# Optimization experiments

Hardware: AMD Instinct MI355X
Metric: run time of the kernel (lower is better)

Reference implementation:

```python
import jax, jax.numpy as jnp
import numpy as np

D_MODEL = 1024
D_STATE = 128
D_CONV = 4
EXPAND = 2
HEADDIM = 64
NGROUPS = 1
CHUNK = 256
D_INNER = EXPAND * D_MODEL          # 2048
NHEADS = D_INNER // HEADDIM         # 32
D_IN_PROJ = 2 * D_INNER + 2 * NGROUPS * D_STATE + NHEADS  # 4384
CONV_DIM = D_INNER + 2 * NGROUPS * D_STATE                # 2304
BATCH, SEQLEN = 2, 2048


def rmsnorm(x, w, eps=1e-6):
    ms = jnp.mean(x * x, axis=-1, keepdims=True)
    return w * (x * jax.lax.rsqrt(ms + eps))


def layernorm(x, eps=1e-5):
    mu = jnp.mean(x, axis=-1, keepdims=True)
    var = jnp.mean((x - mu) ** 2, axis=-1, keepdims=True)
    return (x - mu) * jax.lax.rsqrt(var + eps)


def activation_quant(x):
    # int8-style fake quant with STE, scale differentiable (matches torch)
    amax = jnp.clip(jnp.max(jnp.abs(x), axis=-1, keepdims=True), 1e-5, None)
    scale = 127.0 / amax
    q = jnp.clip(jnp.round(x * scale), -128, 127)
    return (jax.lax.stop_gradient(q - x * scale) + x * scale) / scale


def weight_quant(w):
    # ternary {-1,0,1}; note: NOT rescaled by scale (matches the triton kernel)
    scale = jnp.clip(jnp.mean(jnp.abs(w)), 1e-5, None)
    wq = jnp.clip(jnp.round(w / scale), -1.0, 1.0)
    return w + jax.lax.stop_gradient(wq - w)  # STE: identity grad


def bitlinear(x, w):
    return activation_quant(layernorm(x)) @ weight_quant(w).T


def segsum(x):
    # x: [..., T] -> [..., T, T] lower-triangular cumulative segment sums
    T = x.shape[-1]
    cs = jnp.cumsum(x, axis=-1)
    ss = cs[..., :, None] - cs[..., None, :]
    mask = jnp.tril(jnp.ones((T, T), dtype=bool))
    return jnp.where(mask, ss, -jnp.inf)


def ssd(u, a, B, C, chunk):
    # u: b l h p (= x*dt); a: b l h (= A*dt); B, C: b l h n (per-head)
    b, l, h, p = u.shape
    n = B.shape[-1]
    c = l // chunk
    u = u.reshape(b, c, chunk, h, p)
    a = a.reshape(b, c, chunk, h).transpose(0, 3, 1, 2)   # b h c s
    B = B.reshape(b, c, chunk, h, n)
    C = C.reshape(b, c, chunk, h, n)
    a_cs = jnp.cumsum(a, axis=-1)                          # b h c s
    L = jnp.exp(segsum(a))                                 # b h c s s
    Y_diag = jnp.einsum('bclhn,bcshn,bhcls,bcshp->bclhp', C, B, L, u)
    decay_states = jnp.exp(a_cs[..., -1:] - a_cs)          # b h c s
    states = jnp.einsum('bclhn,bhcl,bclhp->bchpn', B, decay_states, u)
    a_chunk = jnp.pad(a_cs[..., -1], ((0, 0), (0, 0), (1, 0)))  # b h (c+1)
    decay_chunk = jnp.exp(segsum(a_chunk))                 # b h (c+1) (c+1)
    states = jnp.concatenate([jnp.zeros_like(states[:, :1]), states], axis=1)
    new_states = jnp.einsum('bhzc,bchpn->bzhpn', decay_chunk, states)
    prev_states = new_states[:, :-1]                       # state entering each chunk
    Y_off = jnp.einsum('bclhn,bchpn,bhcl->bclhp', C, prev_states, jnp.exp(a_cs))
    return (Y_diag + Y_off).reshape(b, l, h, p)


def setup_inputs() -> dict:
    key = jax.random.key(0)
    ks = jax.random.split(key, 6)
    hidden_states = jax.random.normal(ks[0], (BATCH, SEQLEN, D_MODEL), jnp.float32)
    in_proj_w = jax.random.normal(ks[1], (D_IN_PROJ, D_MODEL), jnp.float32) / np.sqrt(D_MODEL).astype(np.float32)
    out_proj_w = jax.random.normal(ks[2], (D_MODEL, D_INNER), jnp.float32) / np.sqrt(D_INNER).astype(np.float32)
    conv_w = jax.random.normal(ks[3], (CONV_DIM, D_CONV), jnp.float32) * 0.1
    conv_b = jnp.zeros((CONV_DIM,), jnp.float32)
    A_log = jnp.log(jnp.arange(1, NHEADS + 1, dtype=jnp.float32))
    Dp = jnp.ones((NHEADS,), jnp.float32)
    dt_min, dt_max, dt_floor = 1e-3, 1e-1, 1e-4
    inv_dt = jnp.exp(jax.random.uniform(ks[4], (NHEADS,)) * (np.log(dt_max) - np.log(dt_min)) + np.log(dt_min))
    inv_dt = jnp.clip(inv_dt, dt_floor, None)
    dt_bias = inv_dt + jnp.log(-jnp.expm1(-inv_dt))
    norm_w = jnp.ones((D_MODEL,), jnp.float32)
    out_norm_w = jnp.ones((D_INNER,), jnp.float32)
    return dict(hidden_states=hidden_states, norm_w=norm_w, in_proj_w=in_proj_w,
                conv_w=conv_w, conv_b=conv_b, A_log=A_log, Dp=Dp, dt_bias=dt_bias,
                out_norm_w=out_norm_w, out_proj_w=out_proj_w)


def reference(hidden_states, norm_w, in_proj_w, conv_w, conv_b, A_log, Dp, dt_bias, out_norm_w, out_proj_w):
    b, l, _ = hidden_states.shape
    h = rmsnorm(hidden_states, norm_w)
    zxbcdt = bitlinear(h, in_proj_w)                       # b l (2*d_inner + 2*g*n + h)
    z = zxbcdt[..., :D_INNER]
    xBC = zxbcdt[..., D_INNER:D_INNER + CONV_DIM]
    dt = zxbcdt[..., D_INNER + CONV_DIM:]                  # b l h
    # causal depthwise conv1d (kernel D_CONV) + silu
    xp = jnp.pad(xBC, ((0, 0), (D_CONV - 1, 0), (0, 0)))
    conv = sum(xp[:, k:k + l, :] * conv_w[:, k] for k in range(D_CONV)) + conv_b
    xBC = jax.nn.silu(conv)
    x = xBC[..., :D_INNER].reshape(b, l, NHEADS, HEADDIM)
    Bm = xBC[..., D_INNER:D_INNER + NGROUPS * D_STATE].reshape(b, l, NGROUPS, D_STATE)
    Cm = xBC[..., D_INNER + NGROUPS * D_STATE:].reshape(b, l, NGROUPS, D_STATE)
    hpg = NHEADS // NGROUPS
    Bh = jnp.repeat(Bm, hpg, axis=2)                       # b l h n
    Ch = jnp.repeat(Cm, hpg, axis=2)
    dt = jax.nn.softplus(dt + dt_bias)                     # dt_softplus=True
    A = -jnp.exp(A_log)
    y = ssd(x * dt[..., None], dt * A, Bh, Ch, CHUNK)      # b l h p
    y = y + x * Dp[None, None, :, None]                    # D skip
    y = y * jax.nn.silu(z).reshape(b, l, NHEADS, HEADDIM)  # z gate
    y = rmsnorm(y.reshape(b, l, D_INNER), out_norm_w)
    out = bitlinear(y, out_proj_w)
    return hidden_states + out
```

## Files before the change

### kernel.cpp

```cpp
#include <hip/hip_runtime.h>
#include <stdint.h>
#include <stddef.h>
#include <math.h>

#define TOKS 4096
#define DM   1024
#define DIP  4384
#define DI   2048
#define CVD  2304
#define NH   32
#define HD   64
#define DST  128
#define NCH  8
#define CHK  256

typedef int v4i  __attribute__((ext_vector_type(4)));
typedef int v16i __attribute__((ext_vector_type(16)));
typedef short s8v __attribute__((ext_vector_type(8)));
typedef float f16v __attribute__((ext_vector_type(16)));
typedef unsigned short ushort_t;

static const size_t OFF_ZX    = 0;
static const size_t OFF_SX    = OFF_ZX + (size_t)TOKS*DIP*4;
static const size_t OFF_ST    = OFF_SX + (size_t)TOKS*CVD*4;
static const size_t OFF_YG    = OFF_ST + (size_t)512*HD*DST*4;
static const size_t OFF_Q1    = OFF_YG + (size_t)TOKS*DI*4;
static const size_t OFF_Q2    = OFF_Q1 + (size_t)TOKS*DM;
static const size_t OFF_WQ1   = OFF_Q2 + (size_t)TOKS*DI;
static const size_t OFF_WQ2   = OFF_WQ1 + (size_t)DIP*DM;
static const size_t OFF_RS1   = OFF_WQ2 + (size_t)DM*DI;
static const size_t OFF_RS2   = OFF_RS1 + (size_t)TOKS*4;
static const size_t OFF_DT    = OFF_RS2 + (size_t)TOKS*4;
static const size_t OFF_ACS   = OFF_DT + (size_t)TOKS*NH*4;
static const size_t OFF_CSUM  = OFF_ACS + (size_t)512*CHK*8;
static const size_t OFF_PART  = OFF_CSUM + 512*8;
static const size_t OFF_WSC   = OFF_PART + 1024*8;
static const size_t OFF_BH    = OFF_WSC + 64;
static const size_t OFF_BL    = OFF_BH  + (size_t)TOKS*128*2;
static const size_t OFF_CHG   = OFF_BL  + (size_t)TOKS*128*2;
static const size_t OFF_CLG   = OFF_CHG + (size_t)TOKS*128*2;
static const size_t OFF_GRAM  = OFF_CLG + (size_t)TOKS*128*2;
static const size_t OFF_UTH   = OFF_GRAM + (size_t)16*256*256*4;
static const size_t OFF_UTL   = OFF_UTH + (size_t)512*64*256*2;
static const size_t OFF_PH    = OFF_UTL + (size_t)512*64*256*2;
static const size_t OFF_PL    = OFF_PH  + (size_t)512*64*128*2;

__device__ __forceinline__ ushort_t f2bf(float x) {
  union { float f; unsigned int u; } v; v.f = x;
  unsigned int r = v.u + 0x7FFFu + ((v.u >> 16) & 1u);
  return (ushort_t)(r >> 16);
}
__device__ __forceinline__ float bf2f(ushort_t h) {
  union { unsigned int u; float f; } v; v.u = ((unsigned int)h) << 16;
  return v.f;
}

__device__ __forceinline__ double bsumd(double v, double* sb) {
#pragma unroll
  for (int o = 32; o; o >>= 1) v += __shfl_down(v, o);
  int lane = threadIdx.x & 63, w = threadIdx.x >> 6;
  __syncthreads();
  if (lane == 0) sb[w] = v;
  __syncthreads();
  return sb[0] + sb[1] + sb[2] + sb[3];
}
__device__ __forceinline__ double bmaxd(double v, double* sb) {
#pragma unroll
  for (int o = 32; o; o >>= 1) v = fmax(v, __shfl_down(v, o));
  int lane = threadIdx.x & 63, w = threadIdx.x >> 6;
  __syncthreads();
  if (lane == 0) sb[w] = v;
  __syncthreads();
  return fmax(fmax(sb[0], sb[1]), fmax(sb[2], sb[3]));
}
__device__ __forceinline__ void bsum3d(double& a, double& b, double& c, double* sb) {
#pragma unroll
  for (int o = 32; o; o >>= 1) {
    a += __shfl_down(a, o);
    b += __shfl_down(b, o);
    c += __shfl_down(c, o);
  }
  int lane = threadIdx.x & 63, w = threadIdx.x >> 6;
  __syncthreads();
  if (lane == 0) { sb[w * 3 + 0] = a; sb[w * 3 + 1] = b; sb[w * 3 + 2] = c; }
  __syncthreads();
  a = sb[0] + sb[3] + sb[6] + sb[9];
  b = sb[1] + sb[4] + sb[7] + sb[10];
  c = sb[2] + sb[5] + sb[8] + sb[11];
}

__global__ void __launch_bounds__(256) k_absmean(const float* __restrict__ w, int n, double* __restrict__ part) {
  double s = 0.0;
  for (int i = blockIdx.x * 256 + threadIdx.x; i < n; i += 512 * 256) s += (double)fabsf(w[i]);
  __shared__ double sb[4];
  s = bsumd(s, sb);
  if (threadIdx.x == 0) part[blockIdx.x] = s;
}

__global__ void __launch_bounds__(256) k_wscale(const double* __restrict__ part, double* __restrict__ wsc, int n1, int n2) {
  __shared__ double sb[4];
  double s = part[threadIdx.x] + part[threadIdx.x + 256];
  double t1 = bsumd(s, sb);
  __syncthreads();
  s = part[512 + threadIdx.x] + part[512 + threadIdx.x + 256];
  double t2 = bsumd(s, sb);
  if (threadIdx.x == 0) {
    wsc[0] = fmax(t1 / (double)n1, 1e-5);
    wsc[1] = fmax(t2 / (double)n2, 1e-5);
  }
}

__global__ void __launch_bounds__(256) k_tern(const float* __restrict__ w, int n, const double* __restrict__ wsc, int which, int8_t* __restrict__ out) {
  int i = blockIdx.x * 256 + threadIdx.x;
  if (i < n) {
    double sc = wsc[which];
    double q = fmin(fmax(rint((double)w[i] / sc), -1.0), 1.0);
    out[i] = (int8_t)q;
  }
}

template <int D>
__global__ void __launch_bounds__(256) k_normquant(const float* __restrict__ in, const float* __restrict__ w,
                                                   int8_t* __restrict__ q, float* __restrict__ rs) {
  constexpr int E = D / 256;
  int t = blockIdx.x, tid = threadIdx.x;
  const float* row = in + (size_t)t * D;
  __shared__ double sb[12];
  double y[E];
  double s0 = 0.0, s1 = 0.0, s2 = 0.0;
#pragma unroll
  for (int i = 0; i < E; i++) {
    double xv = (double)row[tid + 256 * i];
    double wv = (double)w[tid + 256 * i];
    s0 += xv * xv;
    double yy = wv * xv;
    y[i] = yy;
    s1 += yy;
    s2 += yy * yy;
  }
  bsum3d(s0, s1, s2, sb);
  double rr = 1.0 / sqrt(s0 / (double)D + 1e-6);
  double mu = rr * (s1 / (double)D);
  double var = rr * rr * (s2 / (double)D) - mu * mu;
  double rv = 1.0 / sqrt(var + 1e-5);
  double M = 0.0;
#pragma unroll
  for (int i = 0; i < E; i++) { y[i] = y[i] * rr - mu; M = fmax(M, fabs(y[i])); }
  M = bmaxd(M, sb);
  double am = fmax(M * rv, 1e-5);
  double sc = 127.0 / am;
#pragma unroll
  for (int i = 0; i < E; i++) {
    double qq = fmin(fmax(rint(y[i] * rv * sc), -128.0), 127.0);
    q[(size_t)t * D + tid + 256 * i] = (int8_t)qq;
  }
  if (tid == 0) rs[t] = (float)(am / 127.0);
}

__global__ void __launch_bounds__(256, 3) k_gemm_mfma(const int8_t* __restrict__ A, const int8_t* __restrict__ W,
                                                      const float* __restrict__ rs, const float* __restrict__ addend,
                                                      float* __restrict__ out, int M, int N, int K) {
  __shared__ int8_t Al[128 * 80];
  __shared__ int8_t Bl[128 * 80];
  int m0 = blockIdx.x * 128, n0 = blockIdx.y * 128;
  int t = threadIdx.x;
  int w = t >> 6, lane = t & 63;
  int wm = w >> 1, wn = w & 1;
  int l31 = lane & 31, lh = lane >> 5;

  v16i acc[2][2] = {};

  for (int k0 = 0; k0 < K; k0 += 64) {
    __syncthreads();
#pragma unroll
    for (int it = 0; it < 2; ++it) {
      int c = t + 256 * it;
      int row = c >> 2, kc = (c & 3) * 16;
      int4 av = *(const int4*)(A + (size_t)(m0 + row) * K + k0 + kc);
      *(int4*)(Al + row * 80 + kc) = av;
      int4 bv;
      if (n0 + row < N) bv = *(const int4*)(W + (size_t)(n0 + row) * K + k0 + kc);
      else { bv.x = bv.y = bv.z = bv.w = 0; }
      *(int4*)(Bl + row * 80 + kc) = bv;
    }
    __syncthreads();
#pragma unroll
    for (int ks = 0; ks < 2; ++ks) {
      v4i af[2], bf[2];
#pragma unroll
      for (int tm = 0; tm < 2; ++tm)
        af[tm] = *(const v4i*)(Al + (wm * 64 + tm * 32 + l31) * 80 + ks * 32 + lh * 16);
#pragma unroll
      for (int tn = 0; tn < 2; ++tn)
        bf[tn] = *(const v4i*)(Bl + (wn * 64 + tn * 32 + l31) * 80 + ks * 32 + lh * 16);
#pragma unroll
      for (int tm = 0; tm < 2; ++tm)
#pragma unroll
        for (int tn = 0; tn < 2; ++tn)
          acc[tm][tn] = __builtin_amdgcn_mfma_i32_32x32x32_i8(af[tm], bf[tn], acc[tm][tn], 0, 0, 0);
    }
  }

#pragma unroll
  for (int tm = 0; tm < 2; ++tm)
#pragma unroll
    for (int tn = 0; tn < 2; ++tn) {
      int n = n0 + wn * 64 + tn * 32 + l31;
      if (n < N) {
#pragma unroll
        for (int r = 0; r < 16; ++r) {
          int mrel = (r & 3) + 8 * (r >> 2) + 4 * lh;
          int m = m0 + wm * 64 + tm * 32 + mrel;
          float v = rs[m] * (float)acc[tm][tn][r];
          if (addend) v += addend[(size_t)m * N + n];
          out[(size_t)m * N + n] = v;
        }
      }
    }
}

__global__ void __launch_bounds__(256) k_conv(const float* __restrict__ zx, const float* __restrict__ cw,
                                              const float* __restrict__ cb, float* __restrict__ sx,
                                              ushort_t* __restrict__ bh, ushort_t* __restrict__ bl,
                                              ushort_t* __restrict__ ch, ushort_t* __restrict__ cl) {
  int c = blockIdx.x * 256 + threadIdx.x;
  int t = blockIdx.y;
  int b = t >> 11, l = t & 2047;
  float acc = cb[c];
#pragma unroll
  for (int k = 0; k < 4; k++) {
    int li = l - 3 + k;
    if (li >= 0) acc = fmaf(zx[(size_t)(b * 2048 + li) * DIP + DI + c], cw[c * 4 + k], acc);
  }
  float val = acc / (1.f + expf(-acc));
  sx[(size_t)t * CVD + c] = val;
  if (c >= DI) {
    int idx = c - DI;
    ushort_t hh = f2bf(val);
    ushort_t ll = f2bf(val - bf2f(hh));
    if (idx < 128) {
      bh[(size_t)t * 128 + idx] = hh;
      bl[(size_t)t * 128 + idx] = ll;
    } else {
      ch[(size_t)t * 128 + idx - 128] = hh;
      cl[(size_t)t * 128 + idx - 128] = ll;
    }
  }
}

__global__ void __launch_bounds__(256) k_dt(const float* __restrict__ zx, const float* __restrict__ dt_bias,
                                            float* __restrict__ dtv) {
  int idx = blockIdx.x * 256 + threadIdx.x;
  int t = idx >> 5, h = idx & 31;
  float x = zx[(size_t)t * DIP + (DI + CVD) + h] + dt_bias[h];
  dtv[idx] = fmaxf(x, 0.f) + log1pf(expf(-fabsf(x)));
}

__global__ void __launch_bounds__(256) k_cumsum(const float* __restrict__ dtv, const float* __restrict__ A_log,
                                                double* __restrict__ acs, double* __restrict__ csum) {
  int bid = blockIdx.x;
  int h = bid & 31, bc = bid >> 5;
  int s = threadIdx.x;
  int tok = bc * 256 + s;
  double negA = -exp((double)A_log[h]);
  double a = (double)dtv[tok * 32 + h] * negA;
  __shared__ double buf[256];
  buf[s] = a;
  __syncthreads();
  for (int o = 1; o < 256; o <<= 1) {
    double add = (s >= o) ? buf[s - o] : 0.0;
    __syncthreads();
    buf[s] += add;
    __syncthreads();
  }
  acs[(size_t)bid * 256 + s] = buf[s];
  if (s == 255) csum[bid] = buf[s];
}

__global__ void __launch_bounds__(256) k_gram(const ushort_t* __restrict__ bhg, const ushort_t* __restrict__ blg,
                                              const ushort_t* __restrict__ chg, const ushort_t* __restrict__ clg,
                                              float* __restrict__ gram) {
  int blk = blockIdx.x;
  int bc = blk >> 3, lt = blk & 7;
  int t = threadIdx.x;
  int w = t >> 6, lane = t & 63;
  int l31 = lane & 31, lhf = lane >> 5;
  __shared__ float Gl[4][32 * 36];

  s8v ch[8], cl[8];
  size_t tokA = (size_t)(bc * 256 + lt * 32 + l31) * 128;
#pragma unroll
  for (int ks = 0; ks < 8; ++ks) {
    ch[ks] = *(const s8v*)(chg + tokA + ks * 16 + lhf * 8);
    cl[ks] = *(const s8v*)(clg + tokA + ks * 16 + lhf * 8);
  }
  for (int st = w; st <= lt; st += 4) {
    size_t tokB = (size_t)(bc * 256 + st * 32 + l31) * 128;
    f16v acc = {};
#pragma unroll
    for (int ks = 0; ks < 8; ++ks) {
      s8v bh = *(const s8v*)(bhg + tokB + ks * 16 + lhf * 8);
      s8v bl = *(const s8v*)(blg + tokB + ks * 16 + lhf * 8);
      acc = __builtin_amdgcn_mfma_f32_32x32x16_bf16(ch[ks], bh, acc, 0, 0, 0);
      acc = __builtin_amdgcn_mfma_f32_32x32x16_bf16(ch[ks], bl, acc, 0, 0, 0);
      acc = __builtin_amdgcn_mfma_f32_32x32x16_bf16(cl[ks], bh, acc, 0, 0, 0);
    }
#pragma unroll
    for (int rr = 0; rr < 16; ++rr) {
      int lrow = (rr & 3) + 8 * (rr >> 2) + 4 * lhf;
      Gl[w][lrow * 36 + l31] = acc[rr];
    }
    int lr = lane >> 1, c0 = (lane & 1) * 16;
    float* gdst = gram + ((size_t)bc * 256 + lt * 32 + lr) * 256 + st * 32 + c0;
#pragma unroll
    for (int i = 0; i < 4; ++i)
      *(float4*)(gdst + i * 4) = *(const float4*)(&Gl[w][lr * 36 + c0 + i * 4]);
  }
}

__global__ void __launch_bounds__(256) k_prepuT(const float* __restrict__ sx, const float* __restrict__ dtv,
                                                ushort_t* __restrict__ uth, ushort_t* __restrict__ utl) {
  int r = blockIdx.x;
  int h = r & 31, bc = r >> 5;
  int t = threadIdx.x;
  __shared__ float Xs[64 * 68];
  __shared__ float dts[64];
  for (int slab = 0; slab < 4; ++slab) {
    int s0 = slab * 64;
    if (slab) __syncthreads();
    if (t < 64) dts[t] = dtv[(size_t)(bc * 256 + s0 + t) * 32 + h];
    {
      int s = t >> 2, pg = (t & 3) * 16;
      const float* xr = sx + (size_t)(bc * 256 + s0 + s) * CVD + h * 64 + pg;
      float* dst = &Xs[s * 68 + pg];
#pragma unroll
      for (int i = 0; i < 4; ++i)
        *(float4*)(dst + i * 4) = *(const float4*)(xr + i * 4);
    }
    __syncthreads();
    {
      int p = t >> 2, sg = (t & 3) * 16;
      union { int4 q[2]; ushort_t e[16]; } H, L;
#pragma unroll
      for (int j = 0; j < 16; ++j) {
        float f = Xs[(sg + j) * 68 + p] * dts[sg + j];
        ushort_t hh = f2bf(f);
        H.e[j] = hh;
        L.e[j] = f2bf(f - bf2f(hh));
      }
      size_t base = ((size_t)r * 64 + p) * 256 + s0 + sg;
      *(int4*)(uth + base) = H.q[0];
      *(int4*)(uth + base + 8) = H.q[1];
      *(int4*)(utl + base) = L.q[0];
      *(int4*)(utl + base + 8) = L.q[1];
    }
  }
}

__global__ void __launch_bounds__(256, 4) k_states2(const float* __restrict__ sx, const float* __restrict__ dtv,
                                                    const double* __restrict__ acs, const double* __restrict__ csum,
                                                    float* __restrict__ states) {
  int r = blockIdx.x;
  int h = r & 31, bc = r >> 5;
  int t = threadIdx.x, tx = t & 15, ty = t >> 4;
  __shared__ float du[64 * 68];
  double last = csum[r];
  float acc[4][8] = {};
  for (int s0 = 0; s0 < 256; s0 += 64) {
    __syncthreads();
    {
      int s = t >> 2, pg = (t & 3) * 16;
      int tok = bc * 256 + s0 + s;
      float w = expf((float)(last - acs[(size_t)r * 256 + s0 + s])) * dtv[(size_t)tok * 32 + h];
      const float* xr = sx + (size_t)tok * CVD + h * 64 + pg;
      float* dst = &du[s * 68 + pg];
#pragma unroll
      for (int i = 0; i < 4; i++) {
        float4 v = *(const float4*)(xr + i * 4);
        v.x *= w; v.y *= w; v.z *= w; v.w *= w;
        *(float4*)(dst + i * 4) = v;
      }
    }
    __syncthreads();
#pragma unroll 4
    for (int s = 0; s < 64; s++) {
      int tok = bc * 256 + s0 + s;
      const float* br = sx + (size_t)tok * CVD + DI + ty * 8;
      float4 b0 = *(const float4*)(br);
      float4 b1 = *(const float4*)(br + 4);
      float4 d4 = *(const float4*)(&du[s * 68 + tx * 4]);
      float dd[4] = {d4.x, d4.y, d4.z, d4.w};
      float bv[8] = {b0.x, b0.y, b0.z, b0.w, b1.x, b1.y, b1.z, b1.w};
#pragma unroll
      for (int i = 0; i < 4; i++)
#pragma unroll
        for (int j = 0; j < 8; j++) acc[i][j] = fmaf(dd[i], bv[j], acc[i][j]);
    }
  }
  size_t base = (size_t)r * (HD * DST);
#pragma unroll
  for (int i = 0; i < 4; i++) {
    float4 v0, v1;
    v0.x = acc[i][0]; v0.y = acc[i][1]; v0.z = acc[i][2]; v0.w = acc[i][3];
    v1.x = acc[i][4]; v1.y = acc[i][5]; v1.z = acc[i][6]; v1.w = acc[i][7];
    *(float4*)(states + base + (size_t)(tx * 4 + i) * DST + ty * 8) = v0;
    *(float4*)(states + base + (size_t)(tx * 4 + i) * DST + ty * 8 + 4) = v1;
  }
}

__global__ void __launch_bounds__(256) k_chunkscan(float* __restrict__ states, const double* __restrict__ csum,
                                                   ushort_t* __restrict__ ph, ushort_t* __restrict__ pl) {
  int idx = blockIdx.x * 256 + threadIdx.x;
  int n = idx & 127, p = (idx >> 7) & 63, h = (idx >> 13) & 31, b = idx >> 18;
  float Nv = 0.f;
  for (int c = 0; c < 8; c++) {
    int bid = (b * 8 + c) * 32 + h;
    size_t addr = (size_t)bid * (HD * DST) + p * DST + n;
    float s = states[addr];
    states[addr] = Nv;
    ushort_t hh = f2bf(Nv);
    ph[addr] = hh;
    pl[addr] = f2bf(Nv - bf2f(hh));
    Nv = Nv * expf((float)csum[bid]) + s;
  }
}

__global__ void __launch_bounds__(64) k_y8(const float* __restrict__ sx, const double* __restrict__ acs,
                                           const ushort_t* __restrict__ chg, const ushort_t* __restrict__ clg,
                                           const ushort_t* __restrict__ prevh, const ushort_t* __restrict__ prevl,
                                           const float* __restrict__ gram,
                                           const ushort_t* __restrict__ uth, const ushort_t* __restrict__ utl,
                                           const float* __restrict__ zx, const float* __restrict__ Dp,
                                           float* __restrict__ yg) {
  int myid = (blockIdx.x & 7) * 512 + (blockIdx.x >> 3);
  int r = myid >> 3, lt = myid & 7;
  int h = r & 31, bc = r >> 5;
  int lane = threadIdx.x;
  int l31 = lane & 31, lhf = lane >> 5;
  int lw = lt * 32;
  int lg = lw + l31;
  const double* acsr = acs + (size_t)r * 256;
  double a_l = acsr[lg];

  f16v Yacc[2] = {};
  {
    size_t ca = (size_t)(bc * 256 + lg) * 128;
#pragma unroll
    for (int ks = 0; ks < 8; ++ks) {
      s8v ch = *(const s8v*)(chg + ca + ks * 16 + lhf * 8);
      s8v cl = *(const s8v*)(clg + ca + ks * 16 + lhf * 8);
#pragma unroll
      for (int pt = 0; pt < 2; ++pt) {
        size_t pa = ((size_t)r * 64 + pt * 32 + l31) * 128 + ks * 16 + lhf * 8;
        s8v ph = *(const s8v*)(prevh + pa);
        s8v pl = *(const s8v*)(prevl + pa);
        Yacc[pt] = __builtin_amdgcn_mfma_f32_32x32x16_bf16(ch, ph, Yacc[pt], 0, 0, 0);
        Yacc[pt] = __builtin_amdgcn_mfma_f32_32x32x16_bf16(ch, pl, Yacc[pt], 0, 0, 0);
        Yacc[pt] = __builtin_amdgcn_mfma_f32_32x32x16_bf16(cl, ph, Yacc[pt], 0, 0, 0);
      }
    }
  }
#pragma unroll
  for (int rr = 0; rr < 16; ++rr) {
    int lrow = (rr & 3) + 8 * (rr >> 2) + 4 * lhf;
    float el = expf((float)acsr[lw + lrow]);
    Yacc[0][rr] *= el;
    Yacc[1][rr] *= el;
  }

  const float* gbase = gram + (size_t)(bc * 256 + lg) * 256;
  size_t ub0 = ((size_t)r * 64 + l31) * 256;
  size_t ub1 = ((size_t)r * 64 + 32 + l31) * 256;

  s8v AH[2], AL[2], UH[4], UL[4];
  {
#pragma unroll
    for (int k2 = 0; k2 < 2; ++k2) {
      int sb = k2 * 16 + lhf * 8;
      float4 g0 = *(const float4*)(gbase + sb);
      float4 g1 = *(const float4*)(gbase + sb + 4);
      float gv[8] = {g0.x, g0.y, g0.z, g0.w, g1.x, g1.y, g1.z, g1.w};
      union { s8v v; ushort_t e[8]; } H, L;
#pragma unroll
      for (int j = 0; j < 8; ++j) {
        float v = 0.f;
        if (sb + j <= lg) v = expf((float)(a_l - acsr[sb + j])) * gv[j];
        ushort_t hh = f2bf(v);
        H.e[j] = hh;
        L.e[j] = f2bf(v - bf2f(hh));
      }
      AH[k2] = H.v; AL[k2] = L.v;
      UH[k2 * 2 + 0] = *(const s8v*)(uth + ub0 + sb);
      UH[k2 * 2 + 1] = *(const s8v*)(uth + ub1 + sb);
      UL[k2 * 2 + 0] = *(const s8v*)(utl + ub0 + sb);
      UL[k2 * 2 + 1] = *(const s8v*)(utl + ub1 + sb);
    }
  }

  for (int st = 0; st <= lt; ++st) {
    float4 ng0[2], ng1[2];
    s8v nUH[4], nUL[4];
    bool more = (st < lt);
    int s1 = (st + 1) * 32;
    if (more) {
#pragma unroll
      for (int k2 = 0; k2 < 2; ++k2) {
        int sb = s1 + k2 * 16 + lhf * 8;
        ng0[k2] = *(const float4*)(gbase + sb);
        ng1[k2] = *(const float4*)(gbase + sb + 4);
        nUH[k2 * 2 + 0] = *(const s8v*)(uth + ub0 + sb);
        nUH[k2 * 2 + 1] = *(const s8v*)(uth + ub1 + sb);
        nUL[k2 * 2 + 0] = *(const s8v*)(utl + ub0 + sb);
        nUL[k2 * 2 + 1] = *(const s8v*)(utl + ub1 + sb);
      }
    }
    __builtin_amdgcn_s_setprio(1);
#pragma unroll
    for (int k2 = 0; k2 < 2; ++k2) {
#pragma unroll
      for (int pt = 0; pt < 2; ++pt) {
        Yacc[pt] = __builtin_amdgcn_mfma_f32_32x32x16_bf16(AH[k2], UH[k2 * 2 + pt], Yacc[pt], 0, 0, 0);
        Yacc[pt] = __builtin_amdgcn_mfma_f32_32x32x16_bf16(AH[k2], UL[k2 * 2 + pt], Yacc[pt], 0, 0, 0);
        Yacc[pt] = __builtin_amdgcn_mfma_f32_32x32x16_bf16(AL[k2], UH[k2 * 2 + pt], Yacc[pt], 0, 0, 0);
      }
    }
    __builtin_amdgcn_s_setprio(0);
    if (more) {
#pragma unroll
      for (int k2 = 0; k2 < 2; ++k2) {
        int sb = s1 + k2 * 16 + lhf * 8;
        float gv[8] = {ng0[k2].x, ng0[k2].y, ng0[k2].z, ng0[k2].w,
                       ng1[k2].x, ng1[k2].y, ng1[k2].z, ng1[k2].w};
        union { s8v v; ushort_t e[8]; } H, L;
#pragma unroll
        for (int j = 0; j < 8; ++j) {
          float v = 0.f;
          if (sb + j <= lg) v = expf((float)(a_l - acsr[sb + j])) * gv[j];
          ushort_t hh = f2bf(v);
          H.e[j] = hh;
          L.e[j] = f2bf(v - bf2f(hh));
        }
        AH[k2] = H.v; AL[k2] = L.v;
        UH[k2 * 2 + 0] = nUH[k2 * 2 + 0];
        UH[k2 * 2 + 1] = nUH[k2 * 2 + 1];
        UL[k2 * 2 + 0] = nUL[k2 * 2 + 0];
        UL[k2 * 2 + 1] = nUL[k2 * 2 + 1];
      }
    }
  }

  float dph = Dp[h];
#pragma unroll
  for (int pt = 0; pt < 2; ++pt) {
    int p = pt * 32 + l31;
#pragma unroll
    for (int rr = 0; rr < 16; ++rr) {
      int lrow = (rr & 3) + 8 * (rr >> 2) + 4 * lhf;
      size_t tok = (size_t)(bc * 256 + lw + lrow);
      float xv = sx[tok * CVD + h * 64 + p];
      float zv = zx[tok * DIP + h * 64 + p];
      float y = (Yacc[pt][rr] + xv * dph) * (zv / (1.f + expf(-zv)));
      yg[tok * DI + h * 64 + p] = y;
    }
  }
}

extern "C" void kernel_launch(void* const* d_in, const int* in_sizes, int n_in,
                              void* d_out, int out_size, void* d_ws, size_t ws_size,
                              hipStream_t stream) {
  const float* hidden   = (const float*)d_in[0];
  const float* norm_w   = (const float*)d_in[1];
  const float* in_proj  = (const float*)d_in[2];
  const float* conv_w   = (const float*)d_in[3];
  const float* conv_b   = (const float*)d_in[4];
  const float* A_log    = (const float*)d_in[5];
  const float* Dp       = (const float*)d_in[6];
  const float* dt_bias  = (const float*)d_in[7];
  const float* out_norm = (const float*)d_in[8];
  const float* out_proj = (const float*)d_in[9];
  float* out = (float*)d_out;

  char* ws = (char*)d_ws;
  float*  zx    = (float*)(ws + OFF_ZX);
  float*  sx    = (float*)(ws + OFF_SX);
  float*  st    = (float*)(ws + OFF_ST);
  float*  yg    = (float*)(ws + OFF_YG);
  int8_t* q1    = (int8_t*)(ws + OFF_Q1);
  int8_t* q2    = (int8_t*)(ws + OFF_Q2);
  int8_t* wq1   = (int8_t*)(ws + OFF_WQ1);
  int8_t* wq2   = (int8_t*)(ws + OFF_WQ2);
  float*  rs1   = (float*)(ws + OFF_RS1);
  float*  rs2   = (float*)(ws + OFF_RS2);
  float*  dtv   = (float*)(ws + OFF_DT);
  double* acs   = (double*)(ws + OFF_ACS);
  double* csum  = (double*)(ws + OFF_CSUM);
  double* part  = (double*)(ws + OFF_PART);
  double* wsc   = (double*)(ws + OFF_WSC);
  ushort_t* bhg = (ushort_t*)(ws + OFF_BH);
  ushort_t* blg = (ushort_t*)(ws + OFF_BL);
  ushort_t* chg = (ushort_t*)(ws + OFF_CHG);
  ushort_t* clg = (ushort_t*)(ws + OFF_CLG);
  float*  gram  = (float*)(ws + OFF_GRAM);
  ushort_t* uth = (ushort_t*)(ws + OFF_UTH);
  ushort_t* utl = (ushort_t*)(ws + OFF_UTL);
  ushort_t* pvh = (ushort_t*)(ws + OFF_PH);
  ushort_t* pvl = (ushort_t*)(ws + OFF_PL);

  const int n1 = DIP * DM, n2 = DM * DI;

  hipLaunchKernelGGL(k_absmean, dim3(512), dim3(256), 0, stream, in_proj, n1, part);
  hipLaunchKernelGGL(k_absmean, dim3(512), dim3(256), 0, stream, out_proj, n2, part + 512);
  hipLaunchKernelGGL(k_wscale, dim3(1), dim3(256), 0, stream, part, wsc, n1, n2);
  hipLaunchKernelGGL(k_tern, dim3((n1 + 255) / 256), dim3(256), 0, stream, in_proj, n1, wsc, 0, wq1);
  hipLaunchKernelGGL(k_tern, dim3((n2 + 255) / 256), dim3(256), 0, stream, out_proj, n2, wsc, 1, wq2);
  hipLaunchKernelGGL(k_normquant<DM>, dim3(TOKS), dim3(256), 0, stream, hidden, norm_w, q1, rs1);
  hipLaunchKernelGGL(k_gemm_mfma, dim3(TOKS / 128, (DIP + 127) / 128), dim3(256), 0, stream,
                     q1, wq1, rs1, (const float*)nullptr, zx, TOKS, DIP, DM);
  hipLaunchKernelGGL(k_conv, dim3(CVD / 256, TOKS), dim3(256), 0, stream, zx, conv_w, conv_b, sx,
                     bhg, blg, chg, clg);
  hipLaunchKernelGGL(k_dt, dim3(TOKS * NH / 256), dim3(256), 0, stream, zx, dt_bias, dtv);
  hipLaunchKernelGGL(k_cumsum, dim3(512), dim3(256), 0, stream, dtv, A_log, acs, csum);
  hipLaunchKernelGGL(k_gram, dim3(128), dim3(256), 0, stream, bhg, blg, chg, clg, gram);
  hipLaunchKernelGGL(k_prepuT, dim3(512), dim3(256), 0, stream, sx, dtv, uth, utl);
  hipLaunchKernelGGL(k_states2, dim3(512), dim3(256), 0, stream, sx, dtv, acs, csum, st);
  hipLaunchKernelGGL(k_chunkscan, dim3(2 * NH * HD * DST / 256), dim3(256), 0, stream, st, csum, pvh, pvl);
  hipLaunchKernelGGL(k_y8, dim3(4096), dim3(64), 0, stream, sx, acs, chg, clg, pvh, pvl, gram, uth, utl, zx, Dp, yg);
  hipLaunchKernelGGL(k_normquant<DI>, dim3(TOKS), dim3(256), 0, stream, yg, out_norm, q2, rs2);
  hipLaunchKernelGGL(k_gemm_mfma, dim3(TOKS / 128, DM / 128), dim3(256), 0, stream,
                     q2, wq2, rs2, hidden, out, TOKS, DM, DI);
  (void)in_sizes; (void)n_in; (void)out_size; (void)ws_size;
}
```

Measured before the change: 422.0 us.

## Store SSD operands in MFMA-fragment order and fold dt softplus into cumsum

The producers (conv, gram, prepuT, chunkscan) now write B/C, the Gram matrix, the transposed u and the previous-state operands in a layout that matches the per-lane MFMA fragment order. Each lane's loads in the gram and y kernels then fall in one contiguous 16-byte chunk and neighbouring lanes read neighbouring chunks, replacing strided row accesses. The dt softplus is fused into the cumsum kernel, which removes one launch and one pass over dt. The y kernel also drops its manual software prefetch and setprio scheduling in favour of a plain loop, which may expose more load latency.

```diff
diff --git a/kernel.cpp b/kernel.cpp
--- a/kernel.cpp
+++ b/kernel.cpp
@@ -221,8 +221,8 @@
 
 __global__ void __launch_bounds__(256) k_conv(const float* __restrict__ zx, const float* __restrict__ cw,
                                               const float* __restrict__ cb, float* __restrict__ sx,
-                                              ushort_t* __restrict__ bh, ushort_t* __restrict__ bl,
-                                              ushort_t* __restrict__ ch, ushort_t* __restrict__ cl) {
+                                              ushort_t* __restrict__ bh2, ushort_t* __restrict__ bl2,
+                                              ushort_t* __restrict__ ch2, ushort_t* __restrict__ cl2) {
   int c = blockIdx.x * 256 + threadIdx.x;
   int t = blockIdx.y;
   int b = t >> 11, l = t & 2047;
@@ -238,32 +238,27 @@
     int idx = c - DI;
     ushort_t hh = f2bf(val);
     ushort_t ll = f2bf(val - bf2f(hh));
-    if (idx < 128) {
-      bh[(size_t)t * 128 + idx] = hh;
-      bl[(size_t)t * 128 + idx] = ll;
-    } else {
-      ch[(size_t)t * 128 + idx - 128] = hh;
-      cl[(size_t)t * 128 + idx - 128] = ll;
-    }
-  }
-}
-
-__global__ void __launch_bounds__(256) k_dt(const float* __restrict__ zx, const float* __restrict__ dt_bias,
-                                            float* __restrict__ dtv) {
-  int idx = blockIdx.x * 256 + threadIdx.x;
-  int t = idx >> 5, h = idx & 31;
-  float x = zx[(size_t)t * DIP + (DI + CVD) + h] + dt_bias[h];
-  dtv[idx] = fmaxf(x, 0.f) + log1pf(expf(-fabsf(x)));
-}
-
-__global__ void __launch_bounds__(256) k_cumsum(const float* __restrict__ dtv, const float* __restrict__ A_log,
+    int bc = t >> 8, lt = (t >> 5) & 7, l31 = t & 31;
+    int n = idx & 127;
+    int ks = n >> 4, lhf = (n >> 3) & 1, j = n & 7;
+    size_t o = ((((size_t)(bc * 8 + lt) * 8 + ks) * 2 + lhf) * 32 + l31) * 8 + j;
+    if (idx < 128) { bh2[o] = hh; bl2[o] = ll; }
+    else           { ch2[o] = hh; cl2[o] = ll; }
+  }
+}
+
+__global__ void __launch_bounds__(256) k_cumsum(const float* __restrict__ zx, const float* __restrict__ dt_bias,
+                                                const float* __restrict__ A_log, float* __restrict__ dtv,
                                                 double* __restrict__ acs, double* __restrict__ csum) {
   int bid = blockIdx.x;
   int h = bid & 31, bc = bid >> 5;
   int s = threadIdx.x;
   int tok = bc * 256 + s;
+  float x = zx[(size_t)tok * DIP + (DI + CVD) + h] + dt_bias[h];
+  float dt = fmaxf(x, 0.f) + log1pf(expf(-fabsf(x)));
+  dtv[(size_t)tok * 32 + h] = dt;
   double negA = -exp((double)A_log[h]);
-  double a = (double)dtv[tok * 32 + h] * negA;
+  double a = (double)dt * negA;
   __shared__ double buf[256];
   buf[s] = a;
   __syncthreads();
@@ -277,9 +272,9 @@
   if (s == 255) csum[bid] = buf[s];
 }
 
-__global__ void __launch_bounds__(256) k_gram(const ushort_t* __restrict__ bhg, const ushort_t* __restrict__ blg,
-                                              const ushort_t* __restrict__ chg, const ushort_t* __restrict__ clg,
-                                              float* __restrict__ gram) {
+__global__ void __launch_bounds__(256) k_gram(const ushort_t* __restrict__ bh2, const ushort_t* __restrict__ bl2,
+                                              const ushort_t* __restrict__ ch2, const ushort_t* __restrict__ cl2,
+                                              float* __restrict__ gr2) {
   int blk = blockIdx.x;
   int bc = blk >> 3, lt = blk & 7;
   int t = threadIdx.x;
@@ -288,19 +283,19 @@
   __shared__ float Gl[4][32 * 36];
 
   s8v ch[8], cl[8];
-  size_t tokA = (size_t)(bc * 256 + lt * 32 + l31) * 128;
 #pragma unroll
   for (int ks = 0; ks < 8; ++ks) {
-    ch[ks] = *(const s8v*)(chg + tokA + ks * 16 + lhf * 8);
-    cl[ks] = *(const s8v*)(clg + tokA + ks * 16 + lhf * 8);
+    size_t ca = ((((size_t)(bc * 8 + lt) * 8 + ks) * 2 + lhf) * 32 + l31) * 8;
+    ch[ks] = *(const s8v*)(ch2 + ca);
+    cl[ks] = *(const s8v*)(cl2 + ca);
   }
   for (int st = w; st <= lt; st += 4) {
-    size_t tokB = (size_t)(bc * 256 + st * 32 + l31) * 128;
     f16v acc = {};
 #pragma unroll
     for (int ks = 0; ks < 8; ++ks) {
-      s8v bh = *(const s8v*)(bhg + tokB + ks * 16 + lhf * 8);
-      s8v bl = *(const s8v*)(blg + tokB + ks * 16 + lhf * 8);
+      size_t ba = ((((size_t)(bc * 8 + st) * 8 + ks) * 2 + lhf) * 32 + l31) * 8;
+      s8v bh = *(const s8v*)(bh2 + ba);
+      s8v bl = *(const s8v*)(bl2 + ba);
       acc = __builtin_amdgcn_mfma_f32_32x32x16_bf16(ch[ks], bh, acc, 0, 0, 0);
       acc = __builtin_amdgcn_mfma_f32_32x32x16_bf16(ch[ks], bl, acc, 0, 0, 0);
       acc = __builtin_amdgcn_mfma_f32_32x32x16_bf16(cl[ks], bh, acc, 0, 0, 0);
@@ -310,16 +305,21 @@
       int lrow = (rr & 3) + 8 * (rr >> 2) + 4 * lhf;
       Gl[w][lrow * 36 + l31] = acc[rr];
     }
-    int lr = lane >> 1, c0 = (lane & 1) * 16;
-    float* gdst = gram + ((size_t)bc * 256 + lt * 32 + lr) * 256 + st * 32 + c0;
-#pragma unroll
-    for (int i = 0; i < 4; ++i)
-      *(float4*)(gdst + i * 4) = *(const float4*)(&Gl[w][lr * 36 + c0 + i * 4]);
+#pragma unroll
+    for (int i2 = 0; i2 < 2; ++i2) {
+      int idx = i2 * 2 + lhf;
+      int k2g = idx >> 1, lhf2 = idx & 1;
+      size_t gb = ((((size_t)(bc * 8 + lt) * 8 + st) * 2 + k2g) * 2 + lhf2) * 256 + l31 * 8;
+      float4 a = *(const float4*)(&Gl[w][l31 * 36 + k2g * 16 + lhf2 * 8]);
+      float4 b = *(const float4*)(&Gl[w][l31 * 36 + k2g * 16 + lhf2 * 8 + 4]);
+      *(float4*)(gr2 + gb) = a;
+      *(float4*)(gr2 + gb + 4) = b;
+    }
   }
 }
 
 __global__ void __launch_bounds__(256) k_prepuT(const float* __restrict__ sx, const float* __restrict__ dtv,
-                                                ushort_t* __restrict__ uth, ushort_t* __restrict__ utl) {
+                                                ushort_t* __restrict__ uth2, ushort_t* __restrict__ utl2) {
   int r = blockIdx.x;
   int h = r & 31, bc = r >> 5;
   int t = threadIdx.x;
@@ -338,21 +338,25 @@
         *(float4*)(dst + i * 4) = *(const float4*)(xr + i * 4);
     }
     __syncthreads();
-    {
-      int p = t >> 2, sg = (t & 3) * 16;
-      union { int4 q[2]; ushort_t e[16]; } H, L;
-#pragma unroll
-      for (int j = 0; j < 16; ++j) {
-        float f = Xs[(sg + j) * 68 + p] * dts[sg + j];
+#pragma unroll
+    for (int half = 0; half < 2; ++half) {
+      int it = t + half * 256;
+      int l31 = it & 31, g = it >> 5;
+      int stl = g >> 3, k2 = (g >> 2) & 1, pt = (g >> 1) & 1, lhf = g & 1;
+      int p = pt * 32 + l31;
+      int sb = stl * 32 + k2 * 16 + lhf * 8;
+      union { int4 q; ushort_t e[8]; } H, L;
+#pragma unroll
+      for (int j = 0; j < 8; ++j) {
+        float f = Xs[(sb + j) * 68 + p] * dts[sb + j];
         ushort_t hh = f2bf(f);
         H.e[j] = hh;
         L.e[j] = f2bf(f - bf2f(hh));
       }
-      size_t base = ((size_t)r * 64 + p) * 256 + s0 + sg;
-      *(int4*)(uth + base) = H.q[0];
-      *(int4*)(uth + base + 8) = H.q[1];
-      *(int4*)(utl + base) = L.q[0];
-      *(int4*)(utl + base + 8) = L.q[1];
+      int st = slab * 2 + stl;
+      size_t base = (((((size_t)r * 8 + st) * 2 + k2) * 2 + pt) * 2 + lhf) * 256 + l31 * 8;
+      *(int4*)(uth2 + base) = H.q;
+      *(int4*)(utl2 + base) = L.q;
     }
   }
 }
@@ -409,9 +413,10 @@
 }
 
 __global__ void __launch_bounds__(256) k_chunkscan(float* __restrict__ states, const double* __restrict__ csum,
-                                                   ushort_t* __restrict__ ph, ushort_t* __restrict__ pl) {
+                                                   ushort_t* __restrict__ ph2, ushort_t* __restrict__ pl2) {
   int idx = blockIdx.x * 256 + threadIdx.x;
   int n = idx & 127, p = (idx >> 7) & 63, h = (idx >> 13) & 31, b = idx >> 18;
+  int ks = n >> 4, lhf = (n >> 3) & 1, j = n & 7, pt = p >> 5, l31 = p & 31;
   float Nv = 0.f;
   for (int c = 0; c < 8; c++) {
     int bid = (b * 8 + c) * 32 + h;
@@ -419,17 +424,18 @@
     float s = states[addr];
     states[addr] = Nv;
     ushort_t hh = f2bf(Nv);
-    ph[addr] = hh;
-    pl[addr] = f2bf(Nv - bf2f(hh));
+    size_t o = (((((size_t)bid * 8 + ks) * 2 + pt) * 2 + lhf) * 32 + l31) * 8 + j;
+    ph2[o] = hh;
+    pl2[o] = f2bf(Nv - bf2f(hh));
     Nv = Nv * expf((float)csum[bid]) + s;
   }
 }
 
-__global__ void __launch_bounds__(64) k_y8(const float* __restrict__ sx, const double* __restrict__ acs,
-                                           const ushort_t* __restrict__ chg, const ushort_t* __restrict__ clg,
-                                           const ushort_t* __restrict__ prevh, const ushort_t* __restrict__ prevl,
-                                           const float* __restrict__ gram,
-                                           const ushort_t* __restrict__ uth, const ushort_t* __restrict__ utl,
+__global__ void __launch_bounds__(64) k_y9(const float* __restrict__ sx, const double* __restrict__ acs,
+                                           const ushort_t* __restrict__ ch2, const ushort_t* __restrict__ cl2,
+                                           const ushort_t* __restrict__ ph2, const ushort_t* __restrict__ pl2,
+                                           const float* __restrict__ gr2,
+                                           const ushort_t* __restrict__ uth2, const ushort_t* __restrict__ utl2,
                                            const float* __restrict__ zx, const float* __restrict__ Dp,
                                            float* __restrict__ yg) {
   int myid = (blockIdx.x & 7) * 512 + (blockIdx.x >> 3);
@@ -443,21 +449,19 @@
   double a_l = acsr[lg];
 
   f16v Yacc[2] = {};
-  {
-    size_t ca = (size_t)(bc * 256 + lg) * 128;
-#pragma unroll
-    for (int ks = 0; ks < 8; ++ks) {
-      s8v ch = *(const s8v*)(chg + ca + ks * 16 + lhf * 8);
-      s8v cl = *(const s8v*)(clg + ca + ks * 16 + lhf * 8);
-#pragma unroll
-      for (int pt = 0; pt < 2; ++pt) {
-        size_t pa = ((size_t)r * 64 + pt * 32 + l31) * 128 + ks * 16 + lhf * 8;
-        s8v ph = *(const s8v*)(prevh + pa);
-        s8v pl = *(const s8v*)(prevl + pa);
-        Yacc[pt] = __builtin_amdgcn_mfma_f32_32x32x16_bf16(ch, ph, Yacc[pt], 0, 0, 0);
-        Yacc[pt] = __builtin_amdgcn_mfma_f32_32x32x16_bf16(ch, pl, Yacc[pt], 0, 0, 0);
-        Yacc[pt] = __builtin_amdgcn_mfma_f32_32x32x16_bf16(cl, ph, Yacc[pt], 0, 0, 0);
-      }
+#pragma unroll
+  for (int ks = 0; ks < 8; ++ks) {
+    size_t ca = ((((size_t)(bc * 8 + lt) * 8 + ks) * 2 + lhf) * 32 + l31) * 8;
+    s8v ch = *(const s8v*)(ch2 + ca);
+    s8v cl = *(const s8v*)(cl2 + ca);
+#pragma unroll
+    for (int pt = 0; pt < 2; ++pt) {
+      size_t pa = (((((size_t)r * 8 + ks) * 2 + pt) * 2 + lhf) * 32 + l31) * 8;
+      s8v ph = *(const s8v*)(ph2 + pa);
+      s8v pl = *(const s8v*)(pl2 + pa);
+      Yacc[pt] = __builtin_amdgcn_mfma_f32_32x32x16_bf16(ch, ph, Yacc[pt], 0, 0, 0);
+      Yacc[pt] = __builtin_amdgcn_mfma_f32_32x32x16_bf16(ch, pl, Yacc[pt], 0, 0, 0);
+      Yacc[pt] = __builtin_amdgcn_mfma_f32_32x32x16_bf16(cl, ph, Yacc[pt], 0, 0, 0);
     }
   }
 #pragma unroll
@@ -468,83 +472,31 @@
     Yacc[1][rr] *= el;
   }
 
-  const float* gbase = gram + (size_t)(bc * 256 + lg) * 256;
-  size_t ub0 = ((size_t)r * 64 + l31) * 256;
-  size_t ub1 = ((size_t)r * 64 + 32 + l31) * 256;
-
-  s8v AH[2], AL[2], UH[4], UL[4];
-  {
+  for (int st = 0; st <= lt; ++st) {
 #pragma unroll
     for (int k2 = 0; k2 < 2; ++k2) {
-      int sb = k2 * 16 + lhf * 8;
-      float4 g0 = *(const float4*)(gbase + sb);
-      float4 g1 = *(const float4*)(gbase + sb + 4);
+      size_t gb = (((((size_t)(bc * 8 + lt) * 8 + st) * 2 + k2) * 2 + lhf) * 256) + l31 * 8;
+      float4 g0 = *(const float4*)(gr2 + gb);
+      float4 g1 = *(const float4*)(gr2 + gb + 4);
       float gv[8] = {g0.x, g0.y, g0.z, g0.w, g1.x, g1.y, g1.z, g1.w};
-      union { s8v v; ushort_t e[8]; } H, L;
+      int sbase = st * 32 + k2 * 16 + lhf * 8;
+      union { s8v v; ushort_t e[8]; } AH, AL;
 #pragma unroll
       for (int j = 0; j < 8; ++j) {
         float v = 0.f;
-        if (sb + j <= lg) v = expf((float)(a_l - acsr[sb + j])) * gv[j];
+        if (sbase + j <= lg) v = expf((float)(a_l - acsr[sbase + j])) * gv[j];
         ushort_t hh = f2bf(v);
-        H.e[j] = hh;
-        L.e[j] = f2bf(v - bf2f(hh));
+        AH.e[j] = hh;
+        AL.e[j] = f2bf(v - bf2f(hh));
       }
-      AH[k2] = H.v; AL[k2] = L.v;
-      UH[k2 * 2 + 0] = *(const s8v*)(uth + ub0 + sb);
-      UH[k2 * 2 + 1] = *(const s8v*)(uth + ub1 + sb);
-      UL[k2 * 2 + 0] = *(const s8v*)(utl + ub0 + sb);
-      UL[k2 * 2 + 1] = *(const s8v*)(utl + ub1 + sb);
-    }
-  }
-
-  for (int st = 0; st <= lt; ++st) {
-    float4 ng0[2], ng1[2];
-    s8v nUH[4], nUL[4];
-    bool more = (st < lt);
-    int s1 = (st + 1) * 32;
-    if (more) {
-#pragma unroll
-      for (int k2 = 0; k2 < 2; ++k2) {
-        int sb = s1 + k2 * 16 + lhf * 8;
-        ng0[k2] = *(const float4*)(gbase + sb);
-        ng1[k2] = *(const float4*)(gbase + sb + 4);
-        nUH[k2 * 2 + 0] = *(const s8v*)(uth + ub0 + sb);
-        nUH[k2 * 2 + 1] = *(const s8v*)(uth + ub1 + sb);
-        nUL[k2 * 2 + 0] = *(const s8v*)(utl + ub0 + sb);
-        nUL[k2 * 2 + 1] = *(const s8v*)(utl + ub1 + sb);
-      }
-    }
-    __builtin_amdgcn_s_setprio(1);
-#pragma unroll
-    for (int k2 = 0; k2 < 2; ++k2) {
 #pragma unroll
       for (int pt = 0; pt < 2; ++pt) {
-        Yacc[pt] = __builtin_amdgcn_mfma_f32_32x32x16_bf16(AH[k2], UH[k2 * 2 + pt], Yacc[pt], 0, 0, 0);
-        Yacc[pt] = __builtin_amdgcn_mfma_f32_32x32x16_bf16(AH[k2], UL[k2 * 2 + pt], Yacc[pt], 0, 0, 0);
-        Yacc[pt] = __builtin_amdgcn_mfma_f32_32x32x16_bf16(AL[k2], UH[k2 * 2 + pt], Yacc[pt], 0, 0, 0);
-      }
-    }
-    __builtin_amdgcn_s_setprio(0);
-    if (more) {
-#pragma unroll
-      for (int k2 = 0; k2 < 2; ++k2) {
-        int sb = s1 + k2 * 16 + lhf * 8;
-        float gv[8] = {ng0[k2].x, ng0[k2].y, ng0[k2].z, ng0[k2].w,
-                       ng1[k2].x, ng1[k2].y, ng1[k2].z, ng1[k2].w};
-        union { s8v v; ushort_t e[8]; } H, L;
-#pragma unroll
-        for (int j = 0; j < 8; ++j) {
-          float v = 0.f;
-          if (sb + j <= lg) v = expf((float)(a_l - acsr[sb + j])) * gv[j];
-          ushort_t hh = f2bf(v);
-          H.e[j] = hh;
-          L.e[j] = f2bf(v - bf2f(hh));
-        }
-        AH[k2] = H.v; AL[k2] = L.v;
-        UH[k2 * 2 + 0] = nUH[k2 * 2 + 0];
-        UH[k2 * 2 + 1] = nUH[k2 * 2 + 1];
-        UL[k2 * 2 + 0] = nUL[k2 * 2 + 0];
-        UL[k2 * 2 + 1] = nUL[k2 * 2 + 1];
+        size_t ub = ((((((size_t)r * 8 + st) * 2 + k2) * 2 + pt) * 2 + lhf) * 256) + l31 * 8;
+        s8v uh = *(const s8v*)(uth2 + ub);
+        s8v ul = *(const s8v*)(utl2 + ub);
+        Yacc[pt] = __builtin_amdgcn_mfma_f32_32x32x16_bf16(AH.v, uh, Yacc[pt], 0, 0, 0);
+        Yacc[pt] = __builtin_amdgcn_mfma_f32_32x32x16_bf16(AH.v, ul, Yacc[pt], 0, 0, 0);
+        Yacc[pt] = __builtin_amdgcn_mfma_f32_32x32x16_bf16(AL.v, uh, Yacc[pt], 0, 0, 0);
       }
     }
   }
@@ -596,15 +548,15 @@
   double* csum  = (double*)(ws + OFF_CSUM);
   double* part  = (double*)(ws + OFF_PART);
   double* wsc   = (double*)(ws + OFF_WSC);
-  ushort_t* bhg = (ushort_t*)(ws + OFF_BH);
-  ushort_t* blg = (ushort_t*)(ws + OFF_BL);
-  ushort_t* chg = (ushort_t*)(ws + OFF_CHG);
-  ushort_t* clg = (ushort_t*)(ws + OFF_CLG);
-  float*  gram  = (float*)(ws + OFF_GRAM);
-  ushort_t* uth = (ushort_t*)(ws + OFF_UTH);
-  ushort_t* utl = (ushort_t*)(ws + OFF_UTL);
-  ushort_t* pvh = (ushort_t*)(ws + OFF_PH);
-  ushort_t* pvl = (ushort_t*)(ws + OFF_PL);
+  ushort_t* bh2 = (ushort_t*)(ws + OFF_BH);
+  ushort_t* bl2 = (ushort_t*)(ws + OFF_BL);
+  ushort_t* ch2 = (ushort_t*)(ws + OFF_CHG);
+  ushort_t* cl2 = (ushort_t*)(ws + OFF_CLG);
+  float*  gr2   = (float*)(ws + OFF_GRAM);
+  ushort_t* uth2 = (ushort_t*)(ws + OFF_UTH);
+  ushort_t* utl2 = (ushort_t*)(ws + OFF_UTL);
+  ushort_t* ph2 = (ushort_t*)(ws + OFF_PH);
+  ushort_t* pl2 = (ushort_t*)(ws + OFF_PL);
 
   const int n1 = DIP * DM, n2 = DM * DI;
 
@@ -617,14 +569,13 @@
   hipLaunchKernelGGL(k_gemm_mfma, dim3(TOKS / 128, (DIP + 127) / 128), dim3(256), 0, stream,
                      q1, wq1, rs1, (const float*)nullptr, zx, TOKS, DIP, DM);
   hipLaunchKernelGGL(k_conv, dim3(CVD / 256, TOKS), dim3(256), 0, stream, zx, conv_w, conv_b, sx,
-                     bhg, blg, chg, clg);
-  hipLaunchKernelGGL(k_dt, dim3(TOKS * NH / 256), dim3(256), 0, stream, zx, dt_bias, dtv);
-  hipLaunchKernelGGL(k_cumsum, dim3(512), dim3(256), 0, stream, dtv, A_log, acs, csum);
-  hipLaunchKernelGGL(k_gram, dim3(128), dim3(256), 0, stream, bhg, blg, chg, clg, gram);
-  hipLaunchKernelGGL(k_prepuT, dim3(512), dim3(256), 0, stream, sx, dtv, uth, utl);
+                     bh2, bl2, ch2, cl2);
+  hipLaunchKernelGGL(k_cumsum, dim3(512), dim3(256), 0, stream, zx, dt_bias, A_log, dtv, acs, csum);
+  hipLaunchKernelGGL(k_gram, dim3(128), dim3(256), 0, stream, bh2, bl2, ch2, cl2, gr2);
+  hipLaunchKernelGGL(k_prepuT, dim3(512), dim3(256), 0, stream, sx, dtv, uth2, utl2);
   hipLaunchKernelGGL(k_states2, dim3(512), dim3(256), 0, stream, sx, dtv, acs, csum, st);
-  hipLaunchKernelGGL(k_chunkscan, dim3(2 * NH * HD * DST / 256), dim3(256), 0, stream, st, csum, pvh, pvl);
-  hipLaunchKernelGGL(k_y8, dim3(4096), dim3(64), 0, stream, sx, acs, chg, clg, pvh, pvl, gram, uth, utl, zx, Dp, yg);
+  hipLaunchKernelGGL(k_chunkscan, dim3(2 * NH * HD * DST / 256), dim3(256), 0, stream, st, csum, ph2, pl2);
+  hipLaunchKernelGGL(k_y9, dim3(4096), dim3(64), 0, stream, sx, acs, ch2, cl2, ph2, pl2, gr2, uth2, utl2, zx, Dp, yg);
   hipLaunchKernelGGL(k_normquant<DI>, dim3(TOKS), dim3(256), 0, stream, yg, out_norm, q2, rs2);
   hipLaunchKernelGGL(k_gemm_mfma, dim3(TOKS / 128, DM / 128), dim3(256), 0, stream,
                      q2, wq2, rs2, hidden, out, TOKS, DM, DI);
```

After: 381.9 us. -9.5%, faster.
